# Optimization experiments

Hardware: AMD Instinct MI355X
Metric: run time of the kernel (lower is better)

Reference implementation:

```python
import jax, jax.numpy as jnp
import numpy as np

T, C, H, W, CI = 4, 64, 96, 96, 16
PS, WS, STR0 = 7, 21, 4
KS, KA = 100, 100
SCALE = 10.0


def conv1x1(x, w, b):
    # x: [T,C,H,W], w: [O,C]
    return jnp.einsum('tchw,oc->tohw', x, w) + b[None, :, None, None]


def unfold_clip(x, ps):
    # clipped-boundary unfold: [T,C,H,W] -> [T, H*W, C*ps*ps]
    t, c, h, w = x.shape
    d = jnp.arange(ps)
    ii = jnp.clip(jnp.arange(h)[:, None] + d[None, :], 0, h - 1)  # [H,ps]
    jj = jnp.clip(jnp.arange(w)[:, None] + d[None, :], 0, w - 1)  # [W,ps]
    p = x[:, :, ii]            # [T,C,H,ps,W]
    p = p[:, :, :, :, jj]      # [T,C,H,ps,W,ps]
    p = jnp.transpose(p, (0, 2, 4, 1, 3, 5))  # [T,H,W,C,ps,ps]
    return p.reshape(t, h * w, c * ps * ps)


def setup_inputs() -> dict:
    key = jax.random.key(0)
    ks = jax.random.split(key, 9)
    s = lambda fan: 1.0 / np.sqrt(fan)
    return {
        'vid': jax.random.normal(ks[0], (T, C, H, W), jnp.float32),
        'g_w': jax.random.normal(ks[1], (CI, C), jnp.float32) * s(C),
        'g_b': jax.random.normal(ks[2], (CI,), jnp.float32) * 0.01,
        'theta_w': jax.random.normal(ks[3], (CI, C), jnp.float32) * s(C),
        'theta_b': jax.random.normal(ks[4], (CI,), jnp.float32) * 0.01,
        'phi_w': jax.random.normal(ks[5], (CI, C), jnp.float32) * s(C),
        'phi_b': jax.random.normal(ks[6], (CI,), jnp.float32) * 0.01,
        'W_w': jax.random.normal(ks[7], (C, CI), jnp.float32) * s(CI),
        'W_b': jax.random.normal(ks[8], (C,), jnp.float32) * 0.01,
    }


def reference(vid, g_w, g_b, theta_w, theta_b, phi_w, phi_b, W_w, W_b):
    t, c, h, w = vid.shape
    b1 = conv1x1(vid, g_w, g_b)          # query features  (g)
    b2 = conv1x1(vid, theta_w, theta_b)  # value features  (theta)
    b3 = conv1x1(vid, phi_w, phi_b)      # key features    (phi)

    b1u = unfold_clip(b1, PS)  # [T,HW,D]
    b2u = unfold_clip(b2, PS)
    b3u = unfold_clip(b3, PS)

    # query grid (stride0)
    qi, qj = jnp.meshgrid(jnp.arange(0, h, STR0), jnp.arange(0, w, STR0), indexing='ij')
    qi, qj = qi.reshape(-1), qj.reshape(-1)
    nq = qi.shape[0]
    qflat = qi * w + qj
    b1q = b1u[:, qflat]  # [T,nq,D]

    # centered spatial search window (stride1=1), clipped bounds
    off = jnp.arange(WS) - WS // 2
    ci = jnp.clip(qi[:, None] + off[None, :], 0, h - 1)  # [nq,WS]
    cj = jnp.clip(qj[:, None] + off[None, :], 0, w - 1)
    cand = (ci[:, :, None] * w + cj[:, None, :]).reshape(nq, WS * WS)

    # patch inner-product dists, one window offset at a time (memory-lean)
    def score(cidx):  # cidx: [nq]
        return jnp.einsum('tqd,tqd->tq', b1q, b3u[:, cidx])
    dists = jax.lax.map(score, cand.T)           # [WS*WS,T,nq]
    dists = jnp.transpose(dists, (1, 2, 0))      # [T,nq,WS*WS]

    vals, idx = jax.lax.top_k(dists, KS)
    vals, idx = vals[..., :KA], idx[..., :KA]
    yi = jax.nn.softmax(vals * SCALE, axis=-1)   # [T,nq,KA]

    pos = jnp.take_along_axis(jnp.broadcast_to(cand[None], (t,) + cand.shape), idx, axis=-1)
    patches = b2u[jnp.arange(t)[:, None, None], pos]   # [T,nq,KA,D]
    zi = jnp.einsum('tqk,tqkd->tqd', yi, patches)      # [T,nq,D]

    # fold: overlap-add scatter + counts normalization
    zi = zi.reshape(t, nq, CI, PS, PS).transpose(0, 2, 1, 3, 4).reshape(t, CI, nq * PS * PS)
    d = jnp.arange(PS)
    pi = jnp.clip(qi[:, None] + d[None, :], 0, h - 1)
    pj = jnp.clip(qj[:, None] + d[None, :], 0, w - 1)
    pix = (pi[:, :, None] * w + pj[:, None, :]).reshape(-1)
    acc = jnp.zeros((t, CI, h * w), vid.dtype).at[:, :, pix].add(zi)
    Z = jnp.zeros((h * w,), vid.dtype).at[pix].add(1.0)
    y = (acc / Z).reshape(t, CI, h, w)

    return vid + conv1x1(y, W_w, W_b)
```

## Files before the change

### kernel.cpp

```cpp
#include <hip/hip_runtime.h>
#include <hip/hip_bf16.h>
#include <hip/hip_fp16.h>
#include <math.h>

typedef __hip_bfloat16 bf16;
typedef unsigned int u32;
typedef __attribute__((ext_vector_type(8))) short short8;
typedef __attribute__((ext_vector_type(4))) float float4v;

#define T_   4
#define C_   64
#define H_   96
#define W_   96
#define CI_  16
#define HW_  9216
#define NC_  441
#define K_   100
#define HSEL 0x07060302u
#define LSEL 0x05040100u

__device__ __forceinline__ float ldbf(const void* p, int i) { return __bfloat162float(((const bf16*)p)[i]); }
__device__ __forceinline__ float ldf (const void* p, int i) { return ((const float*)p)[i]; }

__device__ __forceinline__ unsigned short f2bf(float x) {
    union { float f; u32 u; } a; a.f = x;
    u32 r = a.u + 0x7FFF + ((a.u >> 16) & 1);
    return (unsigned short)(r >> 16);
}
__device__ __forceinline__ float bf2f(unsigned short s) {
    union { u32 u; float f; } a; a.u = ((u32)s) << 16;
    return a.f;
}
__device__ __forceinline__ u32 packbf(float x) {
    unsigned short h = f2bf(x);
    unsigned short l = f2bf(x - bf2f(h));
    return ((u32)h << 16) | (u32)l;
}
__device__ __forceinline__ u32 okey(float f) {
    u32 u = __float_as_uint(f);
    return u ^ ((u & 0x80000000u) ? 0xFFFFFFFFu : 0x80000000u);
}
__device__ __forceinline__ float unokey(u32 k) {
    u32 u = (k & 0x80000000u) ? (k ^ 0x80000000u) : ~k;
    return __uint_as_float(u);
}

__device__ __forceinline__ int detect_flag(const void* vid, int tid, int* sflag) {
    if (tid < 64) {
        unsigned short w = ((const unsigned short*)vid)[tid * 2];
        int e = (w >> 7) & 0xFF;
        int sane = ((e >= 100 && e <= 140) || ((w & 0x7FFF) == 0)) ? 1 : 0;
#pragma unroll
        for (int off = 1; off < 64; off <<= 1) sane += __shfl_xor(sane, off);
        if (tid == 0) *sflag = (sane >= 48) ? 1 : 0;
    }
    __syncthreads();
    return *sflag;
}

__global__ __launch_bounds__(256) void conv3_k(const void* vid, const void* gw, const void* gb,
                                               const void* tw, const void* tb, const void* pw,
                                               const void* pb,
                                               u32* __restrict__ B1p, __half* __restrict__ B2h,
                                               u32* __restrict__ B3p, float* __restrict__ ACCb)
{
    __shared__ float w[3120];
    __shared__ int sflag;
    int tid = threadIdx.x;
    int isbf = detect_flag(vid, tid, &sflag);
    if (isbf) {
        for (int i = tid; i < 3120; i += 256) {
            float v;
            if (i < 1024) v = ldbf(gw, i);
            else if (i < 2048) v = ldbf(tw, i - 1024);
            else if (i < 3072) v = ldbf(pw, i - 2048);
            else if (i < 3088) v = ldbf(gb, i - 3072);
            else if (i < 3104) v = ldbf(tb, i - 3088);
            else v = ldbf(pb, i - 3104);
            w[i] = v;
        }
    } else {
        for (int i = tid; i < 3120; i += 256) {
            float v;
            if (i < 1024) v = ldf(gw, i);
            else if (i < 2048) v = ldf(tw, i - 1024);
            else if (i < 3072) v = ldf(pw, i - 2048);
            else if (i < 3088) v = ldf(gb, i - 3072);
            else if (i < 3104) v = ldf(tb, i - 3088);
            else v = ldf(pb, i - 3104);
            w[i] = v;
        }
    }
    __syncthreads();

    {
        float4v z = {0.f, 0.f, 0.f, 0.f};
        *(float4v*)(ACCb + (blockIdx.x * 256 + tid) * 4) = z;
    }

    int lane = tid & 63, og = tid >> 6;
    int g0 = blockIdx.x * 64 + lane;
    int t = g0 / HW_, pix = g0 - t * HW_;

    float a1[4], a2[4], a3[4];
#pragma unroll
    for (int k = 0; k < 4; k++) {
        a1[k] = w[3072 + og * 4 + k];
        a2[k] = w[3088 + og * 4 + k];
        a3[k] = w[3104 + og * 4 + k];
    }
    int base = t * C_ * HW_ + pix;
#pragma unroll 16
    for (int c = 0; c < C_; c++) {
        float v = isbf ? ldbf(vid, base + c * HW_) : ldf(vid, base + c * HW_);
#pragma unroll
        for (int k = 0; k < 4; k++) {
            a1[k] += v * w[(og * 4 + k) * 64 + c];
            a2[k] += v * w[1024 + (og * 4 + k) * 64 + c];
            a3[k] += v * w[2048 + (og * 4 + k) * 64 + c];
        }
    }
    int ob = g0 * 16 + og * 4;
    uint4 p1, p3;
    p1.x = packbf(a1[0]); p1.y = packbf(a1[1]); p1.z = packbf(a1[2]); p1.w = packbf(a1[3]);
    p3.x = packbf(a3[0]); p3.y = packbf(a3[1]); p3.z = packbf(a3[2]); p3.w = packbf(a3[3]);
    *(uint4*)(B1p + ob) = p1;
    *(uint4*)(B3p + ob) = p3;
    __half2 h01 = __floats2half2_rn(a2[0], a2[1]);
    __half2 h23 = __floats2half2_rn(a2[2], a2[3]);
    uint2 p2;
    p2.x = *(u32*)&h01; p2.y = *(u32*)&h23;
    *(uint2*)(B2h + ob) = p2;
}

__global__ __launch_bounds__(256, 4) void attn_k(const u32* __restrict__ B1p,
                                                 const __half* __restrict__ B2h,
                                                 const u32* __restrict__ B3p,
                                                 float* __restrict__ ACCb)
{
    __shared__ __align__(16) char SM[37920];
    short*   Win  = (short*)SM;
    float*   Sc   = (float*)(SM + 28672);
    float*   Cb   = (float*)(SM + 32208);
    int*     hist = (int*)(SM + 32208);
    int*     ctl  = (int*)(SM + 34256);
    float*   red  = (float*)(SM + 34320);
    float*   yiw  = (float*)(SM + 36320);
    int*     pab  = (int*)(SM + 37120);
    __half2* Zc   = (__half2*)(SM + 28672);
    __half2* Wp   = (__half2*)SM;

    int tid = threadIdx.x;
    int p = blockIdx.x, t = blockIdx.y;
    int qy = p / 12, qxp = p - qy * 12;
    int qi = qy * 4, qj = qxp * 8;
    int alo = max(0, 10 - qi), ahi = min(20, 105 - qi);

    const u32*    B1t = B1p + t * HW_ * 16;
    const __half* B2t = B2h + t * HW_ * 16;
    const u32*    B3t = B3p + t * HW_ * 16;

    int lane = tid & 63, wv = tid >> 6;
    int nn = lane & 15, qsel = nn >> 3, pjn = nn & 7;
    int koff = (lane >> 4) * 8;

    short8 Bh[4], Bl[4];
    {
        int qjq = qj + 4 * qsel;
#pragma unroll
        for (int s = 0; s < 4; s++) {
            int kk0 = s * 32 + koff;
            int pi = kk0 >> 4, c0 = kk0 & 15;
            uint4 U0 = {0, 0, 0, 0}, U1 = {0, 0, 0, 0};
            if (pjn < 7 && pi < 7) {
                const u32* src = B1t + (min(qi + pi, 95) * 96 + min(qjq + pjn, 95)) * 16 + c0;
                U0 = *(const uint4*)src;
                U1 = *(const uint4*)(src + 4);
            }
            union { uint4 u; short8 s8; } hc, lc;
            hc.u.x = __builtin_amdgcn_perm(U0.y, U0.x, HSEL);
            hc.u.y = __builtin_amdgcn_perm(U0.w, U0.z, HSEL);
            hc.u.z = __builtin_amdgcn_perm(U1.y, U1.x, HSEL);
            hc.u.w = __builtin_amdgcn_perm(U1.w, U1.z, HSEL);
            lc.u.x = __builtin_amdgcn_perm(U0.y, U0.x, LSEL);
            lc.u.y = __builtin_amdgcn_perm(U0.w, U0.z, LSEL);
            lc.u.z = __builtin_amdgcn_perm(U1.y, U1.x, LSEL);
            lc.u.w = __builtin_amdgcn_perm(U1.w, U1.z, LSEL);
            Bh[s] = hc.s8; Bl[s] = lc.s8;
        }
    }

    for (int pos = tid; pos < 864; pos += 256) {
        int row = pos >> 5, col = pos & 31;
        int vr = min(max(qi - 10 + row, 0), 95);
        int vc = min(max(qj - 10 + col, 0), 95);
        const u32* src = B3t + (vr * 96 + vc) * 16;
        uint4 U0 = *(const uint4*)src,       U1 = *(const uint4*)(src + 4);
        uint4 U2 = *(const uint4*)(src + 8), U3 = *(const uint4*)(src + 12);
        uint4 A, B;
        A.x = __builtin_amdgcn_perm(U0.y, U0.x, HSEL);
        A.y = __builtin_amdgcn_perm(U0.w, U0.z, HSEL);
        A.z = __builtin_amdgcn_perm(U1.y, U1.x, HSEL);
        A.w = __builtin_amdgcn_perm(U1.w, U1.z, HSEL);
        B.x = __builtin_amdgcn_perm(U2.y, U2.x, HSEL);
        B.y = __builtin_amdgcn_perm(U2.w, U2.z, HSEL);
        B.z = __builtin_amdgcn_perm(U3.y, U3.x, HSEL);
        B.w = __builtin_amdgcn_perm(U3.w, U3.z, HSEL);
        *(uint4*)(Win + pos * 16)     = A;
        *(uint4*)(Win + pos * 16 + 8) = B;
    }
    for (int i = tid; i < 512; i += 256) Win[13824 + i] = 0;
    __syncthreads();

    {
        float* Cw = Cb + wv * 256;
        for (int r = wv; r < 21; r += 4) {
            float psum = 0.f;
            int v = (lane >= 21) ? 1 : 0;
            int b = lane - v * 21;
#pragma unroll
            for (int st = 0; st < 2; st++) {
                float4v acc = {0.f, 0.f, 0.f, 0.f};
#pragma unroll
                for (int s = 0; s < 4; s++) {
                    int arow = r + 2 * s + (lane >> 5);
                    int aoff = (arow * 32 + st * 16 + nn) * 16 + ((lane >> 4) & 1) * 8;
                    short8 A = *(const short8*)(Win + aoff);
                    acc = __builtin_amdgcn_mfma_f32_16x16x32_bf16(A, Bh[s], acc, 0, 0, 0);
                    acc = __builtin_amdgcn_mfma_f32_16x16x32_bf16(A, Bl[s], acc, 0, 0, 0);
                }
                *(float4v*)(Cw + nn * 16 + (lane >> 4) * 4) = acc;
                if (lane < 42) {
#pragma unroll
                    for (int pj = 0; pj < 7; pj++) {
                        int sp = b + 4 * v + pj;
                        if ((sp >> 4) == st) psum += Cw[(8 * v + pj) * 16 + (sp & 15)];
                    }
                }
            }
            if (lane < 42) Sc[v * 441 + r * 21 + b] = psum;
        }
    }
    __syncthreads();

    for (int pos = tid; pos < 864; pos += 256) {
        int row = pos >> 5, col = pos & 31;
        int vr = min(max(qi - 10 + row, 0), 95);
        int vc = min(max(qj - 10 + col, 0), 95);
        const u32* src = B3t + (vr * 96 + vc) * 16;
        uint4 U0 = *(const uint4*)src,       U1 = *(const uint4*)(src + 4);
        uint4 U2 = *(const uint4*)(src + 8), U3 = *(const uint4*)(src + 12);
        uint4 A, B;
        A.x = __builtin_amdgcn_perm(U0.y, U0.x, LSEL);
        A.y = __builtin_amdgcn_perm(U0.w, U0.z, LSEL);
        A.z = __builtin_amdgcn_perm(U1.y, U1.x, LSEL);
        A.w = __builtin_amdgcn_perm(U1.w, U1.z, LSEL);
        B.x = __builtin_amdgcn_perm(U2.y, U2.x, LSEL);
        B.y = __builtin_amdgcn_perm(U2.w, U2.z, LSEL);
        B.z = __builtin_amdgcn_perm(U3.y, U3.x, LSEL);
        B.w = __builtin_amdgcn_perm(U3.w, U3.z, LSEL);
        *(uint4*)(Win + pos * 16)     = A;
        *(uint4*)(Win + pos * 16 + 8) = B;
    }
    __syncthreads();

    {
        float* Cw = Cb + wv * 256;
        for (int r = wv; r < 21; r += 4) {
            float psum = 0.f;
            int v = (lane >= 21) ? 1 : 0;
            int b = lane - v * 21;
#pragma unroll
            for (int st = 0; st < 2; st++) {
                float4v acc = {0.f, 0.f, 0.f, 0.f};
#pragma unroll
                for (int s = 0; s < 4; s++) {
                    int arow = r + 2 * s + (lane >> 5);
                    int aoff = (arow * 32 + st * 16 + nn) * 16 + ((lane >> 4) & 1) * 8;
                    short8 A = *(const short8*)(Win + aoff);
                    acc = __builtin_amdgcn_mfma_f32_16x16x32_bf16(A, Bh[s], acc, 0, 0, 0);
                }
                *(float4v*)(Cw + nn * 16 + (lane >> 4) * 4) = acc;
                if (lane < 42) {
#pragma unroll
                    for (int pj = 0; pj < 7; pj++) {
                        int sp = b + 4 * v + pj;
                        if ((sp >> 4) == st) psum += Cw[(8 * v + pj) * 16 + (sp & 15)];
                    }
                }
            }
            if (lane < 42) Sc[v * 441 + r * 21 + b] += psum;
        }
    }
    __syncthreads();

    for (int idx = tid; idx < 882; idx += 256) {
        int v = idx / 441, k = idx - v * 441;
        int a = k / 21, b = k - a * 21;
        int qq = qj + 4 * v;
        int blo = max(0, 10 - qq), bhi = min(20, 105 - qq);
        int ae = min(max(a, alo), ahi), be = min(max(b, blo), bhi);
        if (ae != a || be != b) Sc[v * 441 + k] = Sc[v * 441 + ae * 21 + be];
    }
    for (int pos = tid; pos < 864; pos += 256) {
        int row = pos >> 5, col = pos & 31;
        int vr = min(max(qi - 10 + row, 0), 95);
        int vc = min(max(qj - 10 + col, 0), 95);
        const __half* src = B2t + (vr * 96 + vc) * 16;
        *(int4*)(Wp + pos * 8)     = *(const int4*)src;
        *(int4*)(Wp + pos * 8 + 4) = *(const int4*)(src + 8);
    }
    hist[tid] = 0; hist[256 + tid] = 0;
    if (tid < 16) ctl[tid] = ((tid & 7) == 1) ? K_ : 0;
    __syncthreads();

    int g = tid >> 7, u = tid & 127;
    int wsel = (tid >> 6) & 1;
    u32 kreg[4]; int ni = 0;
    u32 kmax = 0;
    for (int i = u; i < NC_; i += 128) { u32 k = okey(Sc[g * 441 + i]); kmax = max(kmax, k); kreg[ni++] = k; }
#pragma unroll
    for (int off = 1; off < 64; off <<= 1) kmax = max(kmax, (u32)__shfl_xor((int)kmax, off));
    if (lane == 0) red[g * 2 + wsel] = unokey(kmax);

    for (int ps = 3; ps >= 0; ps--) {
        u32 pref = (u32)ctl[g * 8];
        if (!ctl[g * 8 + 3]) {
            for (int a = 0; a < ni; a++) {
                u32 k = kreg[a];
                if (ps == 3 || (k >> ((ps + 1) * 8)) == pref)
                    atomicAdd(&hist[g * 256 + ((k >> (ps * 8)) & 255)], 1);
            }
        }
        __syncthreads();
        if (wv < 2 && !ctl[wv * 8 + 3]) {
            int4 hv = *(int4*)(hist + wv * 256 + lane * 4);
            int local = hv.x + hv.y + hv.z + hv.w;
            int s = local;
#pragma unroll
            for (int off = 1; off < 64; off <<= 1) {
                int tt = __shfl_down(s, off);
                if (lane + off < 64) s += tt;
            }
            int c4 = s - local;
            int c3 = c4 + hv.w, c2 = c3 + hv.z, c1 = c2 + hv.y, c0 = s;
            int need = ctl[wv * 8 + 1];
            u32 pf = (u32)ctl[wv * 8];
            int cums[5] = {c0, c1, c2, c3, c4};
            int hk[4] = {hv.x, hv.y, hv.z, hv.w};
#pragma unroll
            for (int k = 0; k < 4; k++) {
                if (cums[k] >= need && cums[k + 1] < need) {
                    int newneed = need - cums[k + 1];
                    ctl[wv * 8]     = (int)((pf << 8) | (u32)(lane * 4 + k));
                    ctl[wv * 8 + 1] = newneed;
                    if (newneed == hk[k] || ps == 0) { ctl[wv * 8 + 3] = 1; ctl[wv * 8 + 2] = 8 * ps; }
                }
            }
            int4 zz = {0, 0, 0, 0};
            *(int4*)(hist + wv * 256 + lane * 4) = zz;
        }
        __syncthreads();
        if (ctl[3] && ctl[11]) break;
    }

    {
        u32 theta = (u32)ctl[g * 8];
        int shift = ctl[g * 8 + 2];
        int need  = ctl[g * 8 + 1];
        int base  = K_ - need;
        int qq = qj + 4 * g;
        int blo = max(0, 10 - qq), bhi = min(20, 105 - qq);
        int a2 = 0;
        for (int i = u; i < NC_; i += 128) {
            u32 k = kreg[a2++];
            u32 hp = k >> shift;
            int slot = -1;
            if (hp > theta) slot = atomicAdd(&ctl[g * 8 + 4], 1);
            else if (hp == theta) {
                int j = atomicAdd(&ctl[g * 8 + 5], 1);
                if (j < need) slot = base + j;
            }
            if (slot >= 0) {
                int a = i / 21, b = i - a * 21;
                int ae = min(max(a, alo), ahi), be = min(max(b, blo), bhi);
                yiw[g * 100 + slot] = Sc[g * 441 + i];
                pab[g * 100 + slot] = (ae << 8) | (be + 4 * g);
            }
        }
    }
    __syncthreads();
    {
        float m = fmaxf(red[g * 2], red[g * 2 + 1]);
        float wgt = (u < K_) ? expf((yiw[g * 100 + u] - m) * 10.f) : 0.f;
        float pssum = wgt;
#pragma unroll
        for (int off = 1; off < 64; off <<= 1) pssum += __shfl_xor(pssum, off);
        if (lane == 0) red[4 + g * 2 + wsel] = pssum;
        __syncthreads();
        float inv = 1.f / (red[4 + g * 2] + red[4 + g * 2 + 1]);
        if (u < K_) yiw[g * 100 + u] = wgt * inv;
    }
    __syncthreads();

    {
        int qv2 = wv & 1, kh = wv >> 1;
        __half2 z[8];
        int rsel = lane & 1;
        int pi = lane / 7, pj = lane - pi * 7;
        if (lane < 49) {
#pragma unroll
            for (int j = 0; j < 8; j++) z[j] = __float2half2_rn(0.f);
            int kb2 = kh * 50;
            for (int k = kb2; k < kb2 + 50; k++) {
                float y = yiw[qv2 * 100 + k];
                int pp = pab[qv2 * 100 + k];
                int row = (pp >> 8) + pi, col = (pp & 255) + pj;
                const __half2* cell = Wp + (row * 32 + col) * 8;
                int4 A0 = *(const int4*)(cell + rsel * 4);
                int4 A1 = *(const int4*)(cell + 4 - rsel * 4);
                const __half2* pa = (const __half2*)&A0;
                const __half2* pb2 = (const __half2*)&A1;
                __half2 yh = __float2half2_rn(y);
#pragma unroll
                for (int j = 0; j < 4; j++) {
                    z[j]     = __hfma2(pa[j],  yh, z[j]);
                    z[4 + j] = __hfma2(pb2[j], yh, z[4 + j]);
                }
            }
        }
        if (kh == 1 && lane < 49) {
            *(int4*)(Zc + (qv2 * 49 + lane) * 8)     = *(int4*)(z);
            *(int4*)(Zc + (qv2 * 49 + lane) * 8 + 4) = *(int4*)(z + 4);
        }
        __syncthreads();
        if (kh == 0 && lane < 49) {
            const __half2* zo = Zc + (qv2 * 49 + lane) * 8;
#pragma unroll
            for (int j = 0; j < 8; j++) z[j] = __hadd2(z[j], zo[j]);
            int orow = min(qi + pi, 95), ocol = min(qj + 4 * qv2 + pj, 95);
            float* dst = ACCb + t * CI_ * HW_ + orow * 96 + ocol;
            int c0 = rsel * 8, c1 = 8 - c0;
#pragma unroll
            for (int jh = 0; jh < 4; jh++) {
                atomicAdd(dst + (c0 + 2 * jh) * HW_,     __low2float(z[jh]));
                atomicAdd(dst + (c0 + 2 * jh + 1) * HW_, __high2float(z[jh]));
                atomicAdd(dst + (c1 + 2 * jh) * HW_,     __low2float(z[4 + jh]));
                atomicAdd(dst + (c1 + 2 * jh + 1) * HW_, __high2float(z[4 + jh]));
            }
        }
    }
}

__device__ __forceinline__ int cntdim(int x) {
    int c = 0;
#pragma unroll
    for (int pp = 0; pp < 7; pp++) {
        int q = x - pp;
        c += (q >= 0 && q <= 92 && ((q & 3) == 0)) ? 1 : 0;
    }
    if (x == 95) c += 3;
    return c;
}

__global__ __launch_bounds__(256) void out_k(const void* vid, const void* Ww, const void* Wb,
                                             const float* __restrict__ ACCb, void* out)
{
    __shared__ float w[1088];
    __shared__ int sflag;
    int tid = threadIdx.x;
    int isbf = detect_flag(vid, tid, &sflag);
    if (isbf) { for (int i = tid; i < 1088; i += 256) w[i] = (i < 1024) ? ldbf(Ww, i) : ldbf(Wb, i - 1024); }
    else      { for (int i = tid; i < 1088; i += 256) w[i] = (i < 1024) ? ldf (Ww, i) : ldf (Wb, i - 1024); }
    __syncthreads();

    int lane = tid & 63, og = tid >> 6;
    int g0 = blockIdx.x * 64 + lane;
    int t = g0 / HW_, pix = g0 - t * HW_;
    int pi = pix / 96, pj = pix - pi * 96;
    float invz = 1.f / (float)(cntdim(pi) * cntdim(pj));

    float y[CI_];
    int ab = t * CI_ * HW_ + pix;
#pragma unroll
    for (int ci = 0; ci < CI_; ci++) y[ci] = ACCb[ab + ci * HW_] * invz;

    int vb = t * C_ * HW_ + pix;
#pragma unroll
    for (int co = og * 16; co < og * 16 + 16; co++) {
        float s = w[1024 + co];
#pragma unroll
        for (int ci = 0; ci < CI_; ci++) s += w[co * 16 + ci] * y[ci];
        int idx = vb + co * HW_;
        float vv = isbf ? ldbf(vid, idx) : ldf(vid, idx);
        float r = vv + s;
        if (isbf) ((bf16*)out)[idx] = __float2bfloat16(r);
        else      ((float*)out)[idx] = r;
    }
}

extern "C" void kernel_launch(void* const* d_in, const int* in_sizes, int n_in,
                              void* d_out, int out_size, void* d_ws, size_t ws_size,
                              hipStream_t stream)
{
    char* ws = (char*)d_ws;
    u32*    B1p  = (u32*)ws;
    __half* B2h  = (__half*)(ws + 2359296);
    u32*    B3p  = (u32*)(ws + 3538944);
    float*  ACCb = (float*)(ws + 5898240);

    conv3_k<<<dim3(576), dim3(256), 0, stream>>>(d_in[0], d_in[1], d_in[2], d_in[3], d_in[4],
                                                 d_in[5], d_in[6], B1p, B2h, B3p, ACCb);
    attn_k<<<dim3(288, T_), dim3(256), 0, stream>>>(B1p, B2h, B3p, ACCb);
    out_k<<<dim3(576), dim3(256), 0, stream>>>(d_in[0], d_in[7], d_in[8], ACCb, d_out);
}
```

Before: 190.2 us.

## Process 2x2 query tile per attention block sharing one key/value window

Each attention block now handles four queries (two rows by two columns) instead of two, loading a 32x32 window of key and value features once and reusing it across both query rows. Each wave owns one query for top-k selection, softmax and aggregation, which removes the cross-wave reductions and partial-sum exchange through shared memory. The output kernel is also repartitioned to 32 pixels by 8 output channels per thread group with twice as many blocks. In exchange, shared memory grows and the occupancy hint drops from 4 to 3 blocks, the grid halves to 576 blocks, and each wave does the full 100-candidate aggregation serially.

Result: faster. 182.5 us (-4.0%).

```diff
diff --git a/kernel.cpp b/kernel.cpp
--- a/kernel.cpp
+++ b/kernel.cpp
@@ -43,6 +43,16 @@
 __device__ __forceinline__ float unokey(u32 k) {
     u32 u = (k & 0x80000000u) ? (k ^ 0x80000000u) : ~k;
     return __uint_as_float(u);
+}
+__device__ __forceinline__ int cntdim(int x) {
+    int c = 0;
+#pragma unroll
+    for (int pp = 0; pp < 7; pp++) {
+        int q = x - pp;
+        c += (q >= 0 && q <= 92 && ((q & 3) == 0)) ? 1 : 0;
+    }
+    if (x == 95) c += 3;
+    return c;
 }
 
 __device__ __forceinline__ int detect_flag(const void* vid, int tid, int* sflag) {
@@ -133,28 +143,25 @@
     *(uint2*)(B2h + ob) = p2;
 }
 
-__global__ __launch_bounds__(256, 4) void attn_k(const u32* __restrict__ B1p,
+__global__ __launch_bounds__(256, 3) void attn_k(const u32* __restrict__ B1p,
                                                  const __half* __restrict__ B2h,
                                                  const u32* __restrict__ B3p,
                                                  float* __restrict__ ACCb)
 {
-    __shared__ __align__(16) char SM[37920];
+    __shared__ __align__(16) char SM[47248];
     short*   Win  = (short*)SM;
-    float*   Sc   = (float*)(SM + 28672);
-    float*   Cb   = (float*)(SM + 32208);
-    int*     hist = (int*)(SM + 32208);
-    int*     ctl  = (int*)(SM + 34256);
-    float*   red  = (float*)(SM + 34320);
-    float*   yiw  = (float*)(SM + 36320);
-    int*     pab  = (int*)(SM + 37120);
-    __half2* Zc   = (__half2*)(SM + 28672);
+    float*   Sc   = (float*)(SM + 32768);
+    float*   Cb   = (float*)(SM + 39824);
+    int*     hist = (int*)(SM + 39824);
+    float*   yiw  = (float*)(SM + 43920);
+    int*     pab  = (int*)(SM + 45520);
+    int*     ctl  = (int*)(SM + 47120);
     __half2* Wp   = (__half2*)SM;
 
     int tid = threadIdx.x;
-    int p = blockIdx.x, t = blockIdx.y;
-    int qy = p / 12, qxp = p - qy * 12;
-    int qi = qy * 4, qj = qxp * 8;
-    int alo = max(0, 10 - qi), ahi = min(20, 105 - qi);
+    int tile = blockIdx.x, t = blockIdx.y;
+    int qy = tile / 12, qx = tile - qy * 12;
+    int qi = qy * 8, qj = qx * 8;
 
     const u32*    B1t = B1p + t * HW_ * 16;
     const __half* B2t = B2h + t * HW_ * 16;
@@ -164,33 +171,7 @@
     int nn = lane & 15, qsel = nn >> 3, pjn = nn & 7;
     int koff = (lane >> 4) * 8;
 
-    short8 Bh[4], Bl[4];
-    {
-        int qjq = qj + 4 * qsel;
-#pragma unroll
-        for (int s = 0; s < 4; s++) {
-            int kk0 = s * 32 + koff;
-            int pi = kk0 >> 4, c0 = kk0 & 15;
-            uint4 U0 = {0, 0, 0, 0}, U1 = {0, 0, 0, 0};
-            if (pjn < 7 && pi < 7) {
-                const u32* src = B1t + (min(qi + pi, 95) * 96 + min(qjq + pjn, 95)) * 16 + c0;
-                U0 = *(const uint4*)src;
-                U1 = *(const uint4*)(src + 4);
-            }
-            union { uint4 u; short8 s8; } hc, lc;
-            hc.u.x = __builtin_amdgcn_perm(U0.y, U0.x, HSEL);
-            hc.u.y = __builtin_amdgcn_perm(U0.w, U0.z, HSEL);
-            hc.u.z = __builtin_amdgcn_perm(U1.y, U1.x, HSEL);
-            hc.u.w = __builtin_amdgcn_perm(U1.w, U1.z, HSEL);
-            lc.u.x = __builtin_amdgcn_perm(U0.y, U0.x, LSEL);
-            lc.u.y = __builtin_amdgcn_perm(U0.w, U0.z, LSEL);
-            lc.u.z = __builtin_amdgcn_perm(U1.y, U1.x, LSEL);
-            lc.u.w = __builtin_amdgcn_perm(U1.w, U1.z, LSEL);
-            Bh[s] = hc.s8; Bl[s] = lc.s8;
-        }
-    }
-
-    for (int pos = tid; pos < 864; pos += 256) {
+    for (int pos = tid; pos < 1024; pos += 256) {
         int row = pos >> 5, col = pos & 31;
         int vr = min(max(qi - 10 + row, 0), 95);
         int vc = min(max(qj - 10 + col, 0), 95);
@@ -209,10 +190,33 @@
         *(uint4*)(Win + pos * 16)     = A;
         *(uint4*)(Win + pos * 16 + 8) = B;
     }
-    for (int i = tid; i < 512; i += 256) Win[13824 + i] = 0;
-    __syncthreads();
-
-    {
+    __syncthreads();
+
+#pragma unroll 1
+    for (int ri = 0; ri < 2; ri++) {
+        short8 Bh[4], Bl[4];
+        int qiq = qi + 4 * ri, qjq = qj + 4 * qsel;
+#pragma unroll
+        for (int s = 0; s < 4; s++) {
+            int kk0 = s * 32 + koff;
+            int pi = kk0 >> 4, c0 = kk0 & 15;
+            uint4 U0 = {0, 0, 0, 0}, U1 = {0, 0, 0, 0};
+            if (pjn < 7 && pi < 7) {
+                const u32* src = B1t + (min(qiq + pi, 95) * 96 + min(qjq + pjn, 95)) * 16 + c0;
+                U0 = *(const uint4*)src;
+                U1 = *(const uint4*)(src + 4);
+            }
+            union { uint4 u; short8 s8; } hc, lc;
+            hc.u.x = __builtin_amdgcn_perm(U0.y, U0.x, HSEL);
+            hc.u.y = __builtin_amdgcn_perm(U0.w, U0.z, HSEL);
+            hc.u.z = __builtin_amdgcn_perm(U1.y, U1.x, HSEL);
+            hc.u.w = __builtin_amdgcn_perm(U1.w, U1.z, HSEL);
+            lc.u.x = __builtin_amdgcn_perm(U0.y, U0.x, LSEL);
+            lc.u.y = __builtin_amdgcn_perm(U0.w, U0.z, LSEL);
+            lc.u.z = __builtin_amdgcn_perm(U1.y, U1.x, LSEL);
+            lc.u.w = __builtin_amdgcn_perm(U1.w, U1.z, LSEL);
+            Bh[s] = hc.s8; Bl[s] = lc.s8;
+        }
         float* Cw = Cb + wv * 256;
         for (int r = wv; r < 21; r += 4) {
             float psum = 0.f;
@@ -223,7 +227,7 @@
                 float4v acc = {0.f, 0.f, 0.f, 0.f};
 #pragma unroll
                 for (int s = 0; s < 4; s++) {
-                    int arow = r + 2 * s + (lane >> 5);
+                    int arow = 4 * ri + r + 2 * s + (lane >> 5);
                     int aoff = (arow * 32 + st * 16 + nn) * 16 + ((lane >> 4) & 1) * 8;
                     short8 A = *(const short8*)(Win + aoff);
                     acc = __builtin_amdgcn_mfma_f32_16x16x32_bf16(A, Bh[s], acc, 0, 0, 0);
@@ -238,12 +242,12 @@
                     }
                 }
             }
-            if (lane < 42) Sc[v * 441 + r * 21 + b] = psum;
-        }
-    }
-    __syncthreads();
-
-    for (int pos = tid; pos < 864; pos += 256) {
+            if (lane < 42) Sc[(ri * 2 + v) * 441 + r * 21 + b] = psum;
+        }
+    }
+    __syncthreads();
+
+    for (int pos = tid; pos < 1024; pos += 256) {
         int row = pos >> 5, col = pos & 31;
         int vr = min(max(qi - 10 + row, 0), 95);
         int vc = min(max(qj - 10 + col, 0), 95);
@@ -264,7 +268,27 @@
     }
     __syncthreads();
 
-    {
+#pragma unroll 1
+    for (int ri = 0; ri < 2; ri++) {
+        short8 Bh[4];
+        int qiq = qi + 4 * ri, qjq = qj + 4 * qsel;
+#pragma unroll
+        for (int s = 0; s < 4; s++) {
+            int kk0 = s * 32 + koff;
+            int pi = kk0 >> 4, c0 = kk0 & 15;
+            uint4 U0 = {0, 0, 0, 0}, U1 = {0, 0, 0, 0};
+            if (pjn < 7 && pi < 7) {
+                const u32* src = B1t + (min(qiq + pi, 95) * 96 + min(qjq + pjn, 95)) * 16 + c0;
+                U0 = *(const uint4*)src;
+                U1 = *(const uint4*)(src + 4);
+            }
+            union { uint4 u; short8 s8; } hc;
+            hc.u.x = __builtin_amdgcn_perm(U0.y, U0.x, HSEL);
+            hc.u.y = __builtin_amdgcn_perm(U0.w, U0.z, HSEL);
+            hc.u.z = __builtin_amdgcn_perm(U1.y, U1.x, HSEL);
+            hc.u.w = __builtin_amdgcn_perm(U1.w, U1.z, HSEL);
+            Bh[s] = hc.s8;
+        }
         float* Cw = Cb + wv * 256;
         for (int r = wv; r < 21; r += 4) {
             float psum = 0.f;
@@ -275,7 +299,7 @@
                 float4v acc = {0.f, 0.f, 0.f, 0.f};
 #pragma unroll
                 for (int s = 0; s < 4; s++) {
-                    int arow = r + 2 * s + (lane >> 5);
+                    int arow = 4 * ri + r + 2 * s + (lane >> 5);
                     int aoff = (arow * 32 + st * 16 + nn) * 16 + ((lane >> 4) & 1) * 8;
                     short8 A = *(const short8*)(Win + aoff);
                     acc = __builtin_amdgcn_mfma_f32_16x16x32_bf16(A, Bh[s], acc, 0, 0, 0);
@@ -289,20 +313,22 @@
                     }
                 }
             }
-            if (lane < 42) Sc[v * 441 + r * 21 + b] += psum;
-        }
-    }
-    __syncthreads();
-
-    for (int idx = tid; idx < 882; idx += 256) {
-        int v = idx / 441, k = idx - v * 441;
+            if (lane < 42) Sc[(ri * 2 + v) * 441 + r * 21 + b] += psum;
+        }
+    }
+    __syncthreads();
+
+    for (int idx = tid; idx < 1764; idx += 256) {
+        int g = idx / 441, k = idx - g * 441;
         int a = k / 21, b = k - a * 21;
-        int qq = qj + 4 * v;
-        int blo = max(0, 10 - qq), bhi = min(20, 105 - qq);
+        int ri = g >> 1, ci = g & 1;
+        int qiq = qi + 4 * ri, qjq = qj + 4 * ci;
+        int alo = max(0, 10 - qiq), ahi = min(20, 105 - qiq);
+        int blo = max(0, 10 - qjq), bhi = min(20, 105 - qjq);
         int ae = min(max(a, alo), ahi), be = min(max(b, blo), bhi);
-        if (ae != a || be != b) Sc[v * 441 + k] = Sc[v * 441 + ae * 21 + be];
-    }
-    for (int pos = tid; pos < 864; pos += 256) {
+        if (ae != a || be != b) Sc[g * 441 + k] = Sc[g * 441 + ae * 21 + be];
+    }
+    for (int pos = tid; pos < 992; pos += 256) {
         int row = pos >> 5, col = pos & 31;
         int vr = min(max(qi - 10 + row, 0), 95);
         int vc = min(max(qj - 10 + col, 0), 95);
@@ -310,18 +336,20 @@
         *(int4*)(Wp + pos * 8)     = *(const int4*)src;
         *(int4*)(Wp + pos * 8 + 4) = *(const int4*)(src + 8);
     }
-    hist[tid] = 0; hist[256 + tid] = 0;
-    if (tid < 16) ctl[tid] = ((tid & 7) == 1) ? K_ : 0;
-    __syncthreads();
-
-    int g = tid >> 7, u = tid & 127;
-    int wsel = (tid >> 6) & 1;
-    u32 kreg[4]; int ni = 0;
+    hist[tid] = 0; hist[256 + tid] = 0; hist[512 + tid] = 0; hist[768 + tid] = 0;
+    if (tid < 32) ctl[tid] = ((tid & 7) == 1) ? K_ : 0;
+    __syncthreads();
+
+    int g = wv;
+    u32 kreg[7]; int ni = 0;
     u32 kmax = 0;
-    for (int i = u; i < NC_; i += 128) { u32 k = okey(Sc[g * 441 + i]); kmax = max(kmax, k); kreg[ni++] = k; }
+    for (int i = lane; i < NC_; i += 64) {
+        u32 k = okey(Sc[g * 441 + i]);
+        kmax = max(kmax, k);
+        kreg[ni++] = k;
+    }
 #pragma unroll
     for (int off = 1; off < 64; off <<= 1) kmax = max(kmax, (u32)__shfl_xor((int)kmax, off));
-    if (lane == 0) red[g * 2 + wsel] = unokey(kmax);
 
     for (int ps = 3; ps >= 0; ps--) {
         u32 pref = (u32)ctl[g * 8];
@@ -333,8 +361,8 @@
             }
         }
         __syncthreads();
-        if (wv < 2 && !ctl[wv * 8 + 3]) {
-            int4 hv = *(int4*)(hist + wv * 256 + lane * 4);
+        if (!ctl[g * 8 + 3]) {
+            int4 hv = *(int4*)(hist + g * 256 + lane * 4);
             int local = hv.x + hv.y + hv.z + hv.w;
             int s = local;
 #pragma unroll
@@ -344,35 +372,37 @@
             }
             int c4 = s - local;
             int c3 = c4 + hv.w, c2 = c3 + hv.z, c1 = c2 + hv.y, c0 = s;
-            int need = ctl[wv * 8 + 1];
-            u32 pf = (u32)ctl[wv * 8];
+            int need = ctl[g * 8 + 1];
+            u32 pf = (u32)ctl[g * 8];
             int cums[5] = {c0, c1, c2, c3, c4};
             int hk[4] = {hv.x, hv.y, hv.z, hv.w};
 #pragma unroll
             for (int k = 0; k < 4; k++) {
                 if (cums[k] >= need && cums[k + 1] < need) {
                     int newneed = need - cums[k + 1];
-                    ctl[wv * 8]     = (int)((pf << 8) | (u32)(lane * 4 + k));
-                    ctl[wv * 8 + 1] = newneed;
-                    if (newneed == hk[k] || ps == 0) { ctl[wv * 8 + 3] = 1; ctl[wv * 8 + 2] = 8 * ps; }
+                    ctl[g * 8]     = (int)((pf << 8) | (u32)(lane * 4 + k));
+                    ctl[g * 8 + 1] = newneed;
+                    if (newneed == hk[k] || ps == 0) { ctl[g * 8 + 3] = 1; ctl[g * 8 + 2] = 8 * ps; }
                 }
             }
             int4 zz = {0, 0, 0, 0};
-            *(int4*)(hist + wv * 256 + lane * 4) = zz;
+            *(int4*)(hist + g * 256 + lane * 4) = zz;
         }
         __syncthreads();
-        if (ctl[3] && ctl[11]) break;
-    }
-
+        if (ctl[3] && ctl[11] && ctl[19] && ctl[27]) break;
+    }
+
+    int ri = g >> 1, ci = g & 1;
+    int qiq = qi + 4 * ri, qjq = qj + 4 * ci;
     {
         u32 theta = (u32)ctl[g * 8];
         int shift = ctl[g * 8 + 2];
         int need  = ctl[g * 8 + 1];
         int base  = K_ - need;
-        int qq = qj + 4 * g;
-        int blo = max(0, 10 - qq), bhi = min(20, 105 - qq);
+        int alo = max(0, 10 - qiq), ahi = min(20, 105 - qiq);
+        int blo = max(0, 10 - qjq), bhi = min(20, 105 - qjq);
         int a2 = 0;
-        for (int i = u; i < NC_; i += 128) {
+        for (int i = lane; i < NC_; i += 64) {
             u32 k = kreg[a2++];
             u32 hp = k >> shift;
             int slot = -1;
@@ -385,82 +415,55 @@
                 int a = i / 21, b = i - a * 21;
                 int ae = min(max(a, alo), ahi), be = min(max(b, blo), bhi);
                 yiw[g * 100 + slot] = Sc[g * 441 + i];
-                pab[g * 100 + slot] = (ae << 8) | (be + 4 * g);
-            }
-        }
-    }
-    __syncthreads();
+                pab[g * 100 + slot] = ((ae + 4 * ri) << 8) | (be + 4 * ci);
+            }
+        }
+    }
     {
-        float m = fmaxf(red[g * 2], red[g * 2 + 1]);
-        float wgt = (u < K_) ? expf((yiw[g * 100 + u] - m) * 10.f) : 0.f;
-        float pssum = wgt;
-#pragma unroll
-        for (int off = 1; off < 64; off <<= 1) pssum += __shfl_xor(pssum, off);
-        if (lane == 0) red[4 + g * 2 + wsel] = pssum;
-        __syncthreads();
-        float inv = 1.f / (red[4 + g * 2] + red[4 + g * 2 + 1]);
-        if (u < K_) yiw[g * 100 + u] = wgt * inv;
-    }
-    __syncthreads();
-
-    {
-        int qv2 = wv & 1, kh = wv >> 1;
+        float m = unokey(kmax);
+        float wa = expf((yiw[g * 100 + lane] - m) * 10.f);
+        float wb2 = (lane < 36) ? expf((yiw[g * 100 + 64 + lane] - m) * 10.f) : 0.f;
+        float ssum = wa + wb2;
+#pragma unroll
+        for (int off = 1; off < 64; off <<= 1) ssum += __shfl_xor(ssum, off);
+        float inv = 1.f / ssum;
+        yiw[g * 100 + lane] = wa * inv;
+        if (lane < 36) yiw[g * 100 + 64 + lane] = wb2 * inv;
+    }
+
+    if (lane < 49) {
+        int pi = lane / 7, pj = lane - pi * 7;
+        int rsel = lane & 1;
         __half2 z[8];
-        int rsel = lane & 1;
-        int pi = lane / 7, pj = lane - pi * 7;
-        if (lane < 49) {
-#pragma unroll
-            for (int j = 0; j < 8; j++) z[j] = __float2half2_rn(0.f);
-            int kb2 = kh * 50;
-            for (int k = kb2; k < kb2 + 50; k++) {
-                float y = yiw[qv2 * 100 + k];
-                int pp = pab[qv2 * 100 + k];
-                int row = (pp >> 8) + pi, col = (pp & 255) + pj;
-                const __half2* cell = Wp + (row * 32 + col) * 8;
-                int4 A0 = *(const int4*)(cell + rsel * 4);
-                int4 A1 = *(const int4*)(cell + 4 - rsel * 4);
-                const __half2* pa = (const __half2*)&A0;
-                const __half2* pb2 = (const __half2*)&A1;
-                __half2 yh = __float2half2_rn(y);
-#pragma unroll
-                for (int j = 0; j < 4; j++) {
-                    z[j]     = __hfma2(pa[j],  yh, z[j]);
-                    z[4 + j] = __hfma2(pb2[j], yh, z[4 + j]);
-                }
-            }
-        }
-        if (kh == 1 && lane < 49) {
-            *(int4*)(Zc + (qv2 * 49 + lane) * 8)     = *(int4*)(z);
-            *(int4*)(Zc + (qv2 * 49 + lane) * 8 + 4) = *(int4*)(z + 4);
-        }
-        __syncthreads();
-        if (kh == 0 && lane < 49) {
-            const __half2* zo = Zc + (qv2 * 49 + lane) * 8;
-#pragma unroll
-            for (int j = 0; j < 8; j++) z[j] = __hadd2(z[j], zo[j]);
-            int orow = min(qi + pi, 95), ocol = min(qj + 4 * qv2 + pj, 95);
-            float* dst = ACCb + t * CI_ * HW_ + orow * 96 + ocol;
-            int c0 = rsel * 8, c1 = 8 - c0;
-#pragma unroll
-            for (int jh = 0; jh < 4; jh++) {
-                atomicAdd(dst + (c0 + 2 * jh) * HW_,     __low2float(z[jh]));
-                atomicAdd(dst + (c0 + 2 * jh + 1) * HW_, __high2float(z[jh]));
-                atomicAdd(dst + (c1 + 2 * jh) * HW_,     __low2float(z[4 + jh]));
-                atomicAdd(dst + (c1 + 2 * jh + 1) * HW_, __high2float(z[4 + jh]));
-            }
-        }
-    }
-}
-
-__device__ __forceinline__ int cntdim(int x) {
-    int c = 0;
-#pragma unroll
-    for (int pp = 0; pp < 7; pp++) {
-        int q = x - pp;
-        c += (q >= 0 && q <= 92 && ((q & 3) == 0)) ? 1 : 0;
-    }
-    if (x == 95) c += 3;
-    return c;
+#pragma unroll
+        for (int j = 0; j < 8; j++) z[j] = __float2half2_rn(0.f);
+        for (int k = 0; k < K_; k++) {
+            float y = yiw[g * 100 + k];
+            int pp = pab[g * 100 + k];
+            int row = (pp >> 8) + pi, col = (pp & 255) + pj;
+            const __half2* cell = Wp + (row * 32 + col) * 8;
+            int4 A0 = *(const int4*)(cell + rsel * 4);
+            int4 A1 = *(const int4*)(cell + 4 - rsel * 4);
+            const __half2* pa = (const __half2*)&A0;
+            const __half2* pb2 = (const __half2*)&A1;
+            __half2 yh = __float2half2_rn(y);
+#pragma unroll
+            for (int j = 0; j < 4; j++) {
+                z[j]     = __hfma2(pa[j],  yh, z[j]);
+                z[4 + j] = __hfma2(pb2[j], yh, z[4 + j]);
+            }
+        }
+        int orow = min(qiq + pi, 95), ocol = min(qjq + pj, 95);
+        float* dst = ACCb + t * CI_ * HW_ + orow * 96 + ocol;
+        int c0 = rsel * 8, c1 = 8 - c0;
+#pragma unroll
+        for (int jh = 0; jh < 4; jh++) {
+            atomicAdd(dst + (c0 + 2 * jh) * HW_,     __low2float(z[jh]));
+            atomicAdd(dst + (c0 + 2 * jh + 1) * HW_, __high2float(z[jh]));
+            atomicAdd(dst + (c1 + 2 * jh) * HW_,     __low2float(z[4 + jh]));
+            atomicAdd(dst + (c1 + 2 * jh + 1) * HW_, __high2float(z[4 + jh]));
+        }
+    }
 }
 
 __global__ __launch_bounds__(256) void out_k(const void* vid, const void* Ww, const void* Wb,
@@ -474,8 +477,8 @@
     else      { for (int i = tid; i < 1088; i += 256) w[i] = (i < 1024) ? ldf (Ww, i) : ldf (Wb, i - 1024); }
     __syncthreads();
 
-    int lane = tid & 63, og = tid >> 6;
-    int g0 = blockIdx.x * 64 + lane;
+    int lane5 = tid & 31, oct = tid >> 5;
+    int g0 = blockIdx.x * 32 + lane5;
     int t = g0 / HW_, pix = g0 - t * HW_;
     int pi = pix / 96, pj = pix - pi * 96;
     float invz = 1.f / (float)(cntdim(pi) * cntdim(pj));
@@ -487,7 +490,7 @@
 
     int vb = t * C_ * HW_ + pix;
 #pragma unroll
-    for (int co = og * 16; co < og * 16 + 16; co++) {
+    for (int co = oct * 8; co < oct * 8 + 8; co++) {
         float s = w[1024 + co];
 #pragma unroll
         for (int ci = 0; ci < CI_; ci++) s += w[co * 16 + ci] * y[ci];
@@ -511,6 +514,6 @@
 
     conv3_k<<<dim3(576), dim3(256), 0, stream>>>(d_in[0], d_in[1], d_in[2], d_in[3], d_in[4],
                                                  d_in[5], d_in[6], B1p, B2h, B3p, ACCb);
-    attn_k<<<dim3(288, T_), dim3(256), 0, stream>>>(B1p, B2h, B3p, ACCb);
-    out_k<<<dim3(576), dim3(256), 0, stream>>>(d_in[0], d_in[7], d_in[8], ACCb, d_out);
-}
+    attn_k<<<dim3(144, T_), dim3(256), 0, stream>>>(B1p, B2h, B3p, ACCb);
+    out_k<<<dim3(1152), dim3(256), 0, stream>>>(d_in[0], d_in[7], d_in[8], ACCb, d_out);
+}
```
